# Kernel tuning notes

Measured on AMD Instinct MI355X. Metric: run time of the kernel, lower is better.

## Reference

```python
import jax, jax.numpy as jnp
import numpy as np

DIM, H, K, RADIUS = 128, 4, 32, 0.3
DH = DIM // H
N, M = 16384, 4096


def setup_inputs() -> dict:
    key = jax.random.key(0)
    ks = jax.random.split(key, 16)
    s = 0.02
    return {
        "xyz": jax.random.normal(ks[0], (N, 3), jnp.float32),
        "feats": jax.random.normal(ks[1], (N, DIM), jnp.float32),
        "idx_center": jax.random.randint(ks[2], (M,), 0, N, jnp.int64),
        "Wq": jax.random.normal(ks[3], (DIM, DIM), jnp.float32) * s,
        "Wk": jax.random.normal(ks[4], (DIM, DIM), jnp.float32) * s,
        "Wv": jax.random.normal(ks[5], (DIM, DIM), jnp.float32) * s,
        "Wo": jax.random.normal(ks[6], (DIM, DIM), jnp.float32) * s,
        "bo": jnp.zeros((DIM,), jnp.float32),
        "g1": jnp.ones((DIM,), jnp.float32),
        "be1": jnp.zeros((DIM,), jnp.float32),
        "g2": jnp.ones((DIM,), jnp.float32),
        "be2": jnp.zeros((DIM,), jnp.float32),
        "W1": jax.random.normal(ks[7], (4 * DIM, DIM), jnp.float32) * s,
        "b1f": jnp.zeros((4 * DIM,), jnp.float32),
        "W2": jax.random.normal(ks[8], (DIM, 4 * DIM), jnp.float32) * s,
        "b2f": jnp.zeros((DIM,), jnp.float32),
    }


def _layernorm(x, g, b, eps=1e-5):
    mu = x.mean(-1, keepdims=True)
    var = ((x - mu) ** 2).mean(-1, keepdims=True)
    return (x - mu) / jnp.sqrt(var + eps) * g + b


def reference(xyz, feats, idx_center, Wq, Wk, Wv, Wo, bo, g1, be1, g2, be2, W1, b1f, W2, b2f):
    m = idx_center.shape[0]
    c_xyz = xyz[idx_center]          # (M,3)
    c_feat = feats[idx_center]       # (M,DIM)
    # pairwise Euclidean distance (M,N), like torch.cdist
    d2 = (jnp.sum(c_xyz * c_xyz, -1)[:, None] + jnp.sum(xyz * xyz, -1)[None, :]
          - 2.0 * (c_xyz @ xyz.T))
    dist = jnp.sqrt(jnp.maximum(d2, 1e-12))
    mask = dist < RADIUS
    mask = mask.at[jnp.arange(m), idx_center].set(True)  # force self-inclusion
    dmask = jnp.where(mask, dist, jnp.inf)
    neg_d, nbr_idx = jax.lax.top_k(-dmask, K)            # k smallest distances
    nbr_dist = -neg_d
    valid = jnp.isfinite(nbr_dist)                       # (M,K)
    nbr_feats = jnp.where(valid[..., None], feats[nbr_idx], 0.0)  # (M,K,DIM)
    # tiny per-center attention
    q = (c_feat @ Wq.T).reshape(m, H, DH)
    k = (nbr_feats @ Wk.T).reshape(m, K, H, DH).transpose(0, 2, 1, 3)  # (M,H,K,DH)
    v = (nbr_feats @ Wv.T).reshape(m, K, H, DH).transpose(0, 2, 1, 3)
    attn = jnp.einsum('mhd,mhkd->mhk', q * (DH ** -0.5), k)
    attn = jnp.where(valid[:, None, :], attn, -1e9)
    attn = jax.nn.softmax(attn, axis=-1)
    out = jnp.einsum('mhk,mhkd->mhd', attn, v)
    out = out.transpose(0, 2, 1).reshape(m, DIM)  # matches torch transpose(1,2).reshape
    upd = out @ Wo.T + bo
    c_feat = c_feat + _layernorm(upd, g1, be1)
    ffn = jax.nn.relu(c_feat @ W1.T + b1f) @ W2.T + b2f
    c_feat = c_feat + _layernorm(ffn, g2, be2)
    nearest = jnp.argmin(dist, axis=0)            # (N,) nearest center per point
    return feats + c_feat[nearest]
```

## Files before the change

### kernel.cpp

```cpp
#include <hip/hip_runtime.h>
#include <hip/hip_bf16.h>

#define DIMF 128
#define KNBR 32
#define NH 4
#define DH 32
#define RADIUS 0.3f
#define CB 8
#define CAND 256
#define PPB 64
#define TMAIN 512

#define PACK_BLOCKS 60

typedef unsigned long long u64t;

__device__ __forceinline__ void tr4_tile(const float4* __restrict__ in4, float4* __restrict__ out4,
                                         int AI, int BI, int a0, int b0, int t, char* smem) {
    float4(*tile)[33] = (float4(*)[33])smem;
    int tx = t & 31, ty = t >> 5;
    for (int r = ty; r < 32; r += 8) tile[r][tx] = in4[(long)(b0 + r) * AI + a0 + tx];
    __syncthreads();
    for (int r = ty; r < 32; r += 8) out4[(long)(a0 + r) * BI + b0 + tx] = tile[tx][r];
}

__global__ __launch_bounds__(256) void pack_kernel(
    const float* __restrict__ Wq, const float* __restrict__ Wv,
    const float* __restrict__ Wo, const float* __restrict__ W1,
    const float* __restrict__ W2, const float* __restrict__ Wk,
    float4* __restrict__ qp4, float4* __restrict__ vp4, float4* __restrict__ op4,
    float4* __restrict__ w1p4, float4* __restrict__ w2p4, float4* __restrict__ kp4) {
    __shared__ __align__(16) char smem[16896];
    int pk = blockIdx.x, t = threadIdx.x;
    if (pk < 4) {
        tr4_tile((const float4*)Wq, qp4, 32, 128, 0, pk * 32, t, smem);
    } else if (pk < 8) {
        tr4_tile((const float4*)Wv, vp4, 32, 128, 0, (pk - 4) * 32, t, smem);
    } else if (pk < 12) {
        tr4_tile((const float4*)Wo, op4, 32, 128, 0, (pk - 8) * 32, t, smem);
    } else if (pk < 28) {
        tr4_tile((const float4*)W1, w1p4, 32, 512, 0, (pk - 12) * 32, t, smem);
    } else if (pk < 44) {
        int i = pk - 28;
        tr4_tile((const float4*)W2, w2p4, 128, 128, (i >> 2) * 32, (i & 3) * 32, t, smem);
    } else {
        int idx = (pk - 44) * 256 + t;
        int q = idx >> 7, j = idx & 127;
        float4 w;
        w.x = Wk[(long)(4 * q + 0) * DIMF + j];
        w.y = Wk[(long)(4 * q + 1) * DIMF + j];
        w.z = Wk[(long)(4 * q + 2) * DIMF + j];
        w.w = Wk[(long)(4 * q + 3) * DIMF + j];
        kp4[q * DIMF + j] = w;
    }
}

__global__ __launch_bounds__(512, 4) void main_kernel(
    const float* __restrict__ xyz, const float* __restrict__ feats,
    const int* __restrict__ idxc,
    const float4* __restrict__ qp4, const float4* __restrict__ kp4,
    const float4* __restrict__ vp4, const float4* __restrict__ op4,
    const float* __restrict__ bo, const float* __restrict__ g1,
    const float* __restrict__ be1, const float* __restrict__ g2,
    const float* __restrict__ be2, const float4* __restrict__ w1p4,
    const float* __restrict__ b1f, const float4* __restrict__ w2p4,
    const float* __restrict__ b2f, float* __restrict__ cfin,
    int* __restrict__ bestm, int N, int M) {
    __shared__ __align__(16) char smem[32768];
    __shared__ int nbrl[CB][KNBR];
    __shared__ int cnt[CB];

    int t = threadIdx.x;
    int b = blockIdx.x;
    int nAttn = M / CB;

    if (b >= nAttn) {
        float4* cds = (float4*)smem;
        int pt = t >> 3, q = t & 7;
        int n = (b - nAttn) * PPB + pt;
        float px = xyz[3 * n], py = xyz[3 * n + 1], pz = xyz[3 * n + 2];
        float bd0 = INFINITY, bd1 = INFINITY;
        int bm0 = 0, bm1 = 0;
        for (int c0 = 0; c0 < M; c0 += 1024) {
            __syncthreads();
            for (int i = t; i < 1024; i += TMAIN) {
                int ic = idxc[c0 + i];
                float cx = xyz[3 * ic], cy = xyz[3 * ic + 1], cz = xyz[3 * ic + 2];
                cds[i] = make_float4(-2.0f * cx, -2.0f * cy, -2.0f * cz,
                                     (cx * cx + cy * cy) + cz * cz);
            }
            __syncthreads();
#pragma unroll 8
            for (int i = 0; i < 64; ++i) {
                int ci0 = q + (2 * i) * 8, ci1 = q + (2 * i + 1) * 8;
                float4 ca = cds[ci0];
                float4 cb = cds[ci1];
                float sa = fmaf(ca.x, px, fmaf(ca.y, py, fmaf(ca.z, pz, ca.w)));
                float sb = fmaf(cb.x, px, fmaf(cb.y, py, fmaf(cb.z, pz, cb.w)));
                if (sa < bd0) { bd0 = sa; bm0 = c0 + ci0; }
                if (sb < bd1) { bd1 = sb; bm1 = c0 + ci1; }
            }
        }
        if (bd1 < bd0 || (bd1 == bd0 && bm1 < bm0)) { bd0 = bd1; bm0 = bm1; }
#pragma unroll
        for (int o = 1; o < 8; o <<= 1) {
            float obd = __shfl_xor(bd0, o);
            int obm = __shfl_xor(bm0, o);
            if (obd < bd0 || (obd == bd0 && obm < bm0)) { bd0 = obd; bm0 = obm; }
        }
        if (q == 0) bestm[n] = bm0;
        return;
    }

    int m0 = b * CB;

    {
        u64t(*cand)[CAND] = (u64t(*)[CAND])smem;
        if (t < CB) cnt[t] = 0;
        __syncthreads();
        float nx[CB], ny[CB], nz[CB], cw[CB];
#pragma unroll
        for (int tc = 0; tc < CB; ++tc) {
            int ic = idxc[m0 + tc];
            float cx = xyz[3 * ic], cy = xyz[3 * ic + 1], cz = xyz[3 * ic + 2];
            cw[tc] = (cx * cx + cy * cy) + cz * cz;
            nx[tc] = -2.0f * cx; ny[tc] = -2.0f * cy; nz[tc] = -2.0f * cz;
        }
        const float R2 = RADIUS * RADIUS;
        for (int n = t; n < N; n += TMAIN) {
            float x = xyz[3 * n], y = xyz[3 * n + 1], z = xyz[3 * n + 2];
            float pw = (x * x + y * y) + z * z;
            float rhs = R2 - pw;
#pragma unroll
            for (int tc = 0; tc < CB; ++tc) {
                float s = fmaf(nx[tc], x, fmaf(ny[tc], y, fmaf(nz[tc], z, cw[tc])));
                if (s < rhs) {
                    int pos = atomicAdd(&cnt[tc], 1);
                    if (pos < CAND)
                        cand[tc][pos] = (((u64t)__float_as_uint(fmaxf(s + pw, 0.0f))) << 32) | (unsigned)n;
                }
            }
        }
        __syncthreads();
        int w = t >> 6, lane = t & 63;
        {
            int cidx = w;
            int C = cnt[cidx] < CAND ? cnt[cidx] : CAND;
            const u64t* vc = cand[cidx];
            if (C <= 64) {
                u64t mykey = (lane < C) ? vc[lane] : ~0ull;
                int rank = 0;
                for (int j = 0; j < C; ++j) rank += (vc[j] < mykey) ? 1 : 0;
                if (lane < C && rank < KNBR) nbrl[cidx][rank] = (int)(mykey & 0xffffffffu);
                if (lane >= C && lane < KNBR) nbrl[cidx][lane] = -1;
            } else {
                u64t mykey[4];
                int myrank[4];
#pragma unroll
                for (int s = 0; s < 4; ++s) {
                    int i = s * 64 + lane;
                    mykey[s] = (i < C) ? vc[i] : ~0ull;
                    myrank[s] = 0;
                }
                for (int j = 0; j < C; ++j) {
                    u64t kj = vc[j];
#pragma unroll
                    for (int s = 0; s < 4; ++s) myrank[s] += (kj < mykey[s]) ? 1 : 0;
                }
#pragma unroll
                for (int s = 0; s < 4; ++s) {
                    int i = s * 64 + lane;
                    if (i < C && myrank[s] < KNBR) nbrl[cidx][myrank[s]] = (int)(mykey[s] & 0xffffffffu);
                }
            }
        }
    }
    __syncthreads();

    float(*cf)[DIMF] = (float(*)[DIMF])smem;
    float(*cf2)[DIMF] = (float(*)[DIMF])(smem + 4096);
    float(*S1)[4 * DIMF] = (float(*)[4 * DIMF])(smem + 8192);
    float(*S2)[DIMF] = (float(*)[DIMF])(smem + 24576);
    float(*S3)[DIMF] = (float(*)[DIMF])(smem + 28672);

    if (t < 256) {
        int c8t = t >> 5, k32t = t & 31;
        int ic = idxc[m0 + c8t];
        *(float4*)&cf[c8t][k32t * 4] = *(const float4*)&feats[(long)ic * DIMF + k32t * 4];
    }
    __syncthreads();

    {
        int i = t & 127, cpair = (t >> 7) * 2;
        float acc0 = 0.f, acc1 = 0.f;
        for (int jj = 0; jj < 32; ++jj) {
            float4 w = qp4[jj * DIMF + i];
            float4 x0 = *(const float4*)&cf[cpair][jj * 4];
            float4 x1 = *(const float4*)&cf[cpair + 1][jj * 4];
            acc0 += w.x * x0.x + w.y * x0.y + w.z * x0.z + w.w * x0.w;
            acc1 += w.x * x1.x + w.y * x1.y + w.z * x1.z + w.w * x1.w;
        }
        S2[cpair][i] = acc0 * 0.17677669529663687f;
        S2[cpair + 1][i] = acc1 * 0.17677669529663687f;
    }
    __syncthreads();

    {
        int j = t & 127, h = t >> 7;
        float acc[8] = {0.f, 0.f, 0.f, 0.f, 0.f, 0.f, 0.f, 0.f};
        for (int d4 = 0; d4 < 8; ++d4) {
            float4 w = kp4[(h * 8 + d4) * DIMF + j];
#pragma unroll
            for (int c = 0; c < 8; ++c) {
                float4 qv = *(const float4*)&S2[c][h * DH + d4 * 4];
                acc[c] += qv.x * w.x + qv.y * w.y + qv.z * w.z + qv.w * w.w;
            }
        }
#pragma unroll
        for (int c = 0; c < 8; ++c) S1[c][h * DIMF + j] = acc[c];
    }
    __syncthreads();

    {
        int c8 = t >> 6, hh = (t >> 5) & 1, k32 = t & 31;
        int h0 = hh * 2, h1 = hh * 2 + 1;
        int ni = nbrl[c8][k32];
        const float* nrow = feats + (long)(ni < 0 ? 0 : ni) * DIMF;
        float lg0 = 0.f, lg1 = 0.f;
        for (int jj = 0; jj < 32; ++jj) {
            float4 f = *(const float4*)&nrow[jj * 4];
            float4 qa = *(const float4*)&S1[c8][h0 * DIMF + jj * 4];
            float4 qb = *(const float4*)&S1[c8][h1 * DIMF + jj * 4];
            lg0 += f.x * qa.x + f.y * qa.y + f.z * qa.z + f.w * qa.w;
            lg1 += f.x * qb.x + f.y * qb.y + f.z * qb.z + f.w * qb.w;
        }
        if (ni < 0) { lg0 = -1e9f; lg1 = -1e9f; }
        {
            float mx = lg0;
            for (int o = 16; o; o >>= 1) mx = fmaxf(mx, __shfl_xor(mx, o, 32));
            float e = expf(lg0 - mx);
            float s = e;
            for (int o = 16; o; o >>= 1) s += __shfl_xor(s, o, 32);
            S3[c8][h0 * KNBR + k32] = e / s;
        }
        {
            float mx = lg1;
            for (int o = 16; o; o >>= 1) mx = fmaxf(mx, __shfl_xor(mx, o, 32));
            float e = expf(lg1 - mx);
            float s = e;
            for (int o = 16; o; o >>= 1) s += __shfl_xor(s, o, 32);
            S3[c8][h1 * KNBR + k32] = e / s;
        }
    }
    __syncthreads();

    {
        int c8 = t >> 6, hh = (t >> 5) & 1, j32 = t & 31;
        int j4 = j32 * 4;
        int h0 = hh * 2, h1 = hh * 2 + 1;
        float a0x = 0.f, a0y = 0.f, a0z = 0.f, a0w = 0.f;
        float a1x = 0.f, a1y = 0.f, a1z = 0.f, a1w = 0.f;
        for (int k = 0; k < KNBR; ++k) {
            int ni = nbrl[c8][k];
            const float* nrow = feats + (long)(ni < 0 ? 0 : ni) * DIMF;
            float4 f = *(const float4*)&nrow[j4];
            float w0 = S3[c8][h0 * KNBR + k], w1 = S3[c8][h1 * KNBR + k];
            a0x += w0 * f.x; a0y += w0 * f.y; a0z += w0 * f.z; a0w += w0 * f.w;
            a1x += w1 * f.x; a1y += w1 * f.y; a1z += w1 * f.z; a1w += w1 * f.w;
        }
        __syncthreads();
        *(float4*)&S1[c8][h0 * DIMF + j4] = make_float4(a0x, a0y, a0z, a0w);
        *(float4*)&S1[c8][h1 * DIMF + j4] = make_float4(a1x, a1y, a1z, a1w);
    }
    __syncthreads();

    {
        int i = t & 127, cpair = (t >> 7) * 2;
        int h = i >> 5, d = i & 31;
        float acc0 = 0.f, acc1 = 0.f;
        for (int jj = 0; jj < 32; ++jj) {
            float4 w = vp4[jj * DIMF + i];
            float4 p0 = *(const float4*)&S1[cpair][h * DIMF + jj * 4];
            float4 p1 = *(const float4*)&S1[cpair + 1][h * DIMF + jj * 4];
            acc0 += w.x * p0.x + w.y * p0.y + w.z * p0.z + w.w * p0.w;
            acc1 += w.x * p1.x + w.y * p1.y + w.z * p1.z + w.w * p1.w;
        }
        __syncthreads();
        S2[cpair][d * NH + h] = acc0;
        S2[cpair + 1][d * NH + h] = acc1;
    }
    __syncthreads();

    {
        int i = t & 127, cpair = (t >> 7) * 2;
        float acc0 = 0.f, acc1 = 0.f;
        for (int jj = 0; jj < 32; ++jj) {
            float4 w = op4[jj * DIMF + i];
            float4 x0 = *(const float4*)&S2[cpair][jj * 4];
            float4 x1 = *(const float4*)&S2[cpair + 1][jj * 4];
            acc0 += w.x * x0.x + w.y * x0.y + w.z * x0.z + w.w * x0.w;
            acc1 += w.x * x1.x + w.y * x1.y + w.z * x1.z + w.w * x1.w;
        }
        float bb = bo[i];
        __syncthreads();
        S3[cpair][i] = acc0 + bb;
        S3[cpair + 1][i] = acc1 + bb;
    }
    __syncthreads();

    if (t < 256) {
        int c8 = t >> 5, k32 = t & 31;
        int i4 = k32 * 4;
        float4 u = *(const float4*)&S3[c8][i4];
        float s = ((u.x + u.y) + u.z) + u.w;
        for (int o = 16; o; o >>= 1) s += __shfl_xor(s, o, 32);
        float mu = s * (1.0f / DIMF);
        float d0 = u.x - mu, d1 = u.y - mu, d2 = u.z - mu, d3 = u.w - mu;
        float vs = ((d0 * d0 + d1 * d1) + d2 * d2) + d3 * d3;
        for (int o = 16; o; o >>= 1) vs += __shfl_xor(vs, o, 32);
        float rs = 1.0f / sqrtf(vs * (1.0f / DIMF) + 1e-5f);
        float4 g = *(const float4*)&g1[i4];
        float4 b = *(const float4*)&be1[i4];
        float4 base = *(const float4*)&cf[c8][i4];
        float4 r;
        r.x = base.x + d0 * rs * g.x + b.x;
        r.y = base.y + d1 * rs * g.y + b.y;
        r.z = base.z + d2 * rs * g.z + b.z;
        r.w = base.w + d3 * rs * g.w + b.w;
        *(float4*)&cf2[c8][i4] = r;
    }
    __syncthreads();

    {
        int u0 = t & 127, p = t >> 7;
        int u = p * DIMF + u0;
        float acc[8] = {0.f, 0.f, 0.f, 0.f, 0.f, 0.f, 0.f, 0.f};
        for (int jj = 0; jj < 32; ++jj) {
            float4 w = w1p4[jj * 512 + u];
#pragma unroll
            for (int c = 0; c < 8; ++c) {
                float4 x = *(const float4*)&cf2[c][jj * 4];
                acc[c] += w.x * x.x + w.y * x.y + w.z * x.z + w.w * x.w;
            }
        }
        float bb = b1f[u];
#pragma unroll
        for (int c = 0; c < 8; ++c) S1[c][u] = fmaxf(acc[c] + bb, 0.f);
    }
    __syncthreads();

    {
        int i = t & 127, cpair = (t >> 7) * 2;
        float acc0 = 0.f, acc1 = 0.f;
        for (int uu = 0; uu < 128; ++uu) {
            float4 w = w2p4[uu * DIMF + i];
            float4 h0v = *(const float4*)&S1[cpair][uu * 4];
            float4 h1v = *(const float4*)&S1[cpair + 1][uu * 4];
            acc0 += w.x * h0v.x + w.y * h0v.y + w.z * h0v.z + w.w * h0v.w;
            acc1 += w.x * h1v.x + w.y * h1v.y + w.z * h1v.z + w.w * h1v.w;
        }
        float bb = b2f[i];
        __syncthreads();
        S3[cpair][i] = acc0 + bb;
        S3[cpair + 1][i] = acc1 + bb;
    }
    __syncthreads();

    if (t < 256) {
        int c8 = t >> 5, k32 = t & 31;
        int i4 = k32 * 4;
        float4 u = *(const float4*)&S3[c8][i4];
        float s = ((u.x + u.y) + u.z) + u.w;
        for (int o = 16; o; o >>= 1) s += __shfl_xor(s, o, 32);
        float mu = s * (1.0f / DIMF);
        float d0 = u.x - mu, d1 = u.y - mu, d2 = u.z - mu, d3 = u.w - mu;
        float vs = ((d0 * d0 + d1 * d1) + d2 * d2) + d3 * d3;
        for (int o = 16; o; o >>= 1) vs += __shfl_xor(vs, o, 32);
        float rs = 1.0f / sqrtf(vs * (1.0f / DIMF) + 1e-5f);
        float4 g = *(const float4*)&g2[i4];
        float4 b = *(const float4*)&be2[i4];
        float4 base = *(const float4*)&cf2[c8][i4];
        float4 r;
        r.x = base.x + d0 * rs * g.x + b.x;
        r.y = base.y + d1 * rs * g.y + b.y;
        r.z = base.z + d2 * rs * g.z + b.z;
        r.w = base.w + d3 * rs * g.w + b.w;
        *(float4*)&cfin[(long)(m0 + c8) * DIMF + i4] = r;
    }
}

__global__ __launch_bounds__(256) void out_kernel(const float4* __restrict__ feats4,
                                                  const float* __restrict__ cfin,
                                                  const int* __restrict__ bestm,
                                                  float4* __restrict__ out4, int total) {
    int idx = blockIdx.x * 256 + threadIdx.x;
    if (idx >= total) return;
    int n = idx >> 5, c = idx & 31;
    const float4* cf4 = (const float4*)cfin;
    float4 f = feats4[idx];
    float4 g = cf4[(long)bestm[n] * 32 + c];
    out4[idx] = make_float4(f.x + g.x, f.y + g.y, f.z + g.z, f.w + g.w);
}

extern "C" void kernel_launch(void* const* d_in, const int* in_sizes, int n_in,
                              void* d_out, int out_size, void* d_ws, size_t ws_size,
                              hipStream_t stream) {
    const float* xyz = (const float*)d_in[0];
    const float* feats = (const float*)d_in[1];
    const int* idxc = (const int*)d_in[2];
    const float* Wq = (const float*)d_in[3];
    const float* Wk = (const float*)d_in[4];
    const float* Wv = (const float*)d_in[5];
    const float* Wo = (const float*)d_in[6];
    const float* bo = (const float*)d_in[7];
    const float* g1 = (const float*)d_in[8];
    const float* be1 = (const float*)d_in[9];
    const float* g2 = (const float*)d_in[10];
    const float* be2 = (const float*)d_in[11];
    const float* W1 = (const float*)d_in[12];
    const float* b1f = (const float*)d_in[13];
    const float* W2 = (const float*)d_in[14];
    const float* b2f = (const float*)d_in[15];

    int N = in_sizes[0] / 3;
    int M = in_sizes[2];

    char* ws = (char*)d_ws;
    size_t off = 0;
    float* cfin = (float*)(ws + off); off += (size_t)M * DIMF * 4;
    int* bestm = (int*)(ws + off); off += (size_t)N * 4;
    float4* qp4 = (float4*)(ws + off); off += (size_t)DIMF * DIMF * 4;
    float4* vp4 = (float4*)(ws + off); off += (size_t)DIMF * DIMF * 4;
    float4* op4 = (float4*)(ws + off); off += (size_t)DIMF * DIMF * 4;
    float4* kp4 = (float4*)(ws + off); off += (size_t)DIMF * DIMF * 4;
    float4* w1p4 = (float4*)(ws + off); off += (size_t)4 * DIMF * DIMF * 4;
    float4* w2p4 = (float4*)(ws + off); off += (size_t)4 * DIMF * DIMF * 4;
    (void)ws_size; (void)n_in; (void)out_size;

    pack_kernel<<<PACK_BLOCKS, 256, 0, stream>>>(
        Wq, Wv, Wo, W1, W2, Wk, qp4, vp4, op4, w1p4, w2p4, kp4);
    main_kernel<<<M / CB + N / PPB, TMAIN, 0, stream>>>(
        xyz, feats, idxc, qp4, kp4, vp4, op4, bo, g1, be1, g2, be2,
        w1p4, b1f, w2p4, b2f, cfin, bestm, N, M);
    out_kernel<<<(N * DIMF / 4 + 255) / 256, 256, 0, stream>>>(
        (const float4*)feats, cfin, bestm, (float4*)d_out, N * DIMF / 4);
}
```

Before: 192.8 us.

## Halve main kernel block to 4 centers and 256 threads

Shrinks each attention block from 8 centers with 512 threads to 4 centers with 256 threads, halves shared memory, and halves points per block in the nearest-center path. The K-projection and FFN1 loops are remapped so each thread covers two heads or two hidden slices to keep full coverage with fewer threads. The aim is more blocks, better CU load balance and lighter per-block sync. The cost is half the weight reuse per block, so each weight element is fetched twice as often from cache.

Result: slower. 204.5 us (+6.1%).

```diff
diff --git a/kernel.cpp b/kernel.cpp
--- a/kernel.cpp
+++ b/kernel.cpp
@@ -6,10 +6,10 @@
 #define NH 4
 #define DH 32
 #define RADIUS 0.3f
-#define CB 8
+#define CB 4
 #define CAND 256
-#define PPB 64
-#define TMAIN 512
+#define PPB 32
+#define TMAIN 256
 
 #define PACK_BLOCKS 60
 
@@ -55,7 +55,7 @@
     }
 }
 
-__global__ __launch_bounds__(512, 4) void main_kernel(
+__global__ __launch_bounds__(256) void main_kernel(
     const float* __restrict__ xyz, const float* __restrict__ feats,
     const int* __restrict__ idxc,
     const float4* __restrict__ qp4, const float4* __restrict__ kp4,
@@ -66,7 +66,7 @@
     const float* __restrict__ b1f, const float4* __restrict__ w2p4,
     const float* __restrict__ b2f, float* __restrict__ cfin,
     int* __restrict__ bestm, int N, int M) {
-    __shared__ __align__(16) char smem[32768];
+    __shared__ __align__(16) char smem[16384];
     __shared__ int nbrl[CB][KNBR];
     __shared__ int cnt[CB];
 
@@ -178,15 +178,15 @@
     __syncthreads();
 
     float(*cf)[DIMF] = (float(*)[DIMF])smem;
-    float(*cf2)[DIMF] = (float(*)[DIMF])(smem + 4096);
-    float(*S1)[4 * DIMF] = (float(*)[4 * DIMF])(smem + 8192);
-    float(*S2)[DIMF] = (float(*)[DIMF])(smem + 24576);
-    float(*S3)[DIMF] = (float(*)[DIMF])(smem + 28672);
-
-    if (t < 256) {
-        int c8t = t >> 5, k32t = t & 31;
-        int ic = idxc[m0 + c8t];
-        *(float4*)&cf[c8t][k32t * 4] = *(const float4*)&feats[(long)ic * DIMF + k32t * 4];
+    float(*cf2)[DIMF] = (float(*)[DIMF])(smem + 2048);
+    float(*S1)[4 * DIMF] = (float(*)[4 * DIMF])(smem + 4096);
+    float(*S2)[DIMF] = (float(*)[DIMF])(smem + 12288);
+    float(*S3)[DIMF] = (float(*)[DIMF])(smem + 14336);
+
+    if (t < 128) {
+        int c4 = t >> 5, k32 = t & 31;
+        int ic = idxc[m0 + c4];
+        *(float4*)&cf[c4][k32 * 4] = *(const float4*)&feats[(long)ic * DIMF + k32 * 4];
     }
     __syncthreads();
 
@@ -206,31 +206,35 @@
     __syncthreads();
 
     {
-        int j = t & 127, h = t >> 7;
-        float acc[8] = {0.f, 0.f, 0.f, 0.f, 0.f, 0.f, 0.f, 0.f};
-        for (int d4 = 0; d4 < 8; ++d4) {
-            float4 w = kp4[(h * 8 + d4) * DIMF + j];
-#pragma unroll
-            for (int c = 0; c < 8; ++c) {
-                float4 qv = *(const float4*)&S2[c][h * DH + d4 * 4];
-                acc[c] += qv.x * w.x + qv.y * w.y + qv.z * w.z + qv.w * w.w;
-            }
-        }
-#pragma unroll
-        for (int c = 0; c < 8; ++c) S1[c][h * DIMF + j] = acc[c];
-    }
-    __syncthreads();
-
-    {
-        int c8 = t >> 6, hh = (t >> 5) & 1, k32 = t & 31;
+        int j = t & 127, hbase = (t >> 7) * 2;
+#pragma unroll
+        for (int hh = 0; hh < 2; ++hh) {
+            int h = hbase + hh;
+            float acc[CB] = {0.f, 0.f, 0.f, 0.f};
+            for (int d4 = 0; d4 < 8; ++d4) {
+                float4 w = kp4[(h * 8 + d4) * DIMF + j];
+#pragma unroll
+                for (int c = 0; c < CB; ++c) {
+                    float4 qv = *(const float4*)&S2[c][h * DH + d4 * 4];
+                    acc[c] += qv.x * w.x + qv.y * w.y + qv.z * w.z + qv.w * w.w;
+                }
+            }
+#pragma unroll
+            for (int c = 0; c < CB; ++c) S1[c][h * DIMF + j] = acc[c];
+        }
+    }
+    __syncthreads();
+
+    {
+        int c4 = t >> 6, hh = (t >> 5) & 1, k32 = t & 31;
         int h0 = hh * 2, h1 = hh * 2 + 1;
-        int ni = nbrl[c8][k32];
+        int ni = nbrl[c4][k32];
         const float* nrow = feats + (long)(ni < 0 ? 0 : ni) * DIMF;
         float lg0 = 0.f, lg1 = 0.f;
         for (int jj = 0; jj < 32; ++jj) {
             float4 f = *(const float4*)&nrow[jj * 4];
-            float4 qa = *(const float4*)&S1[c8][h0 * DIMF + jj * 4];
-            float4 qb = *(const float4*)&S1[c8][h1 * DIMF + jj * 4];
+            float4 qa = *(const float4*)&S1[c4][h0 * DIMF + jj * 4];
+            float4 qb = *(const float4*)&S1[c4][h1 * DIMF + jj * 4];
             lg0 += f.x * qa.x + f.y * qa.y + f.z * qa.z + f.w * qa.w;
             lg1 += f.x * qb.x + f.y * qb.y + f.z * qb.z + f.w * qb.w;
         }
@@ -241,7 +245,7 @@
             float e = expf(lg0 - mx);
             float s = e;
             for (int o = 16; o; o >>= 1) s += __shfl_xor(s, o, 32);
-            S3[c8][h0 * KNBR + k32] = e / s;
+            S3[c4][h0 * KNBR + k32] = e / s;
         }
         {
             float mx = lg1;
@@ -249,28 +253,28 @@
             float e = expf(lg1 - mx);
             float s = e;
             for (int o = 16; o; o >>= 1) s += __shfl_xor(s, o, 32);
-            S3[c8][h1 * KNBR + k32] = e / s;
-        }
-    }
-    __syncthreads();
-
-    {
-        int c8 = t >> 6, hh = (t >> 5) & 1, j32 = t & 31;
+            S3[c4][h1 * KNBR + k32] = e / s;
+        }
+    }
+    __syncthreads();
+
+    {
+        int c4 = t >> 6, hh = (t >> 5) & 1, j32 = t & 31;
         int j4 = j32 * 4;
         int h0 = hh * 2, h1 = hh * 2 + 1;
         float a0x = 0.f, a0y = 0.f, a0z = 0.f, a0w = 0.f;
         float a1x = 0.f, a1y = 0.f, a1z = 0.f, a1w = 0.f;
         for (int k = 0; k < KNBR; ++k) {
-            int ni = nbrl[c8][k];
+            int ni = nbrl[c4][k];
             const float* nrow = feats + (long)(ni < 0 ? 0 : ni) * DIMF;
             float4 f = *(const float4*)&nrow[j4];
-            float w0 = S3[c8][h0 * KNBR + k], w1 = S3[c8][h1 * KNBR + k];
+            float w0 = S3[c4][h0 * KNBR + k], w1 = S3[c4][h1 * KNBR + k];
             a0x += w0 * f.x; a0y += w0 * f.y; a0z += w0 * f.z; a0w += w0 * f.w;
             a1x += w1 * f.x; a1y += w1 * f.y; a1z += w1 * f.z; a1w += w1 * f.w;
         }
         __syncthreads();
-        *(float4*)&S1[c8][h0 * DIMF + j4] = make_float4(a0x, a0y, a0z, a0w);
-        *(float4*)&S1[c8][h1 * DIMF + j4] = make_float4(a1x, a1y, a1z, a1w);
+        *(float4*)&S1[c4][h0 * DIMF + j4] = make_float4(a0x, a0y, a0z, a0w);
+        *(float4*)&S1[c4][h1 * DIMF + j4] = make_float4(a1x, a1y, a1z, a1w);
     }
     __syncthreads();
 
@@ -308,10 +312,10 @@
     }
     __syncthreads();
 
-    if (t < 256) {
-        int c8 = t >> 5, k32 = t & 31;
+    if (t < 128) {
+        int c4 = t >> 5, k32 = t & 31;
         int i4 = k32 * 4;
-        float4 u = *(const float4*)&S3[c8][i4];
+        float4 u = *(const float4*)&S3[c4][i4];
         float s = ((u.x + u.y) + u.z) + u.w;
         for (int o = 16; o; o >>= 1) s += __shfl_xor(s, o, 32);
         float mu = s * (1.0f / DIMF);
@@ -321,31 +325,43 @@
         float rs = 1.0f / sqrtf(vs * (1.0f / DIMF) + 1e-5f);
         float4 g = *(const float4*)&g1[i4];
         float4 b = *(const float4*)&be1[i4];
-        float4 base = *(const float4*)&cf[c8][i4];
+        float4 base = *(const float4*)&cf[c4][i4];
         float4 r;
         r.x = base.x + d0 * rs * g.x + b.x;
         r.y = base.y + d1 * rs * g.y + b.y;
         r.z = base.z + d2 * rs * g.z + b.z;
         r.w = base.w + d3 * rs * g.w + b.w;
-        *(float4*)&cf2[c8][i4] = r;
-    }
-    __syncthreads();
-
-    {
-        int u0 = t & 127, p = t >> 7;
-        int u = p * DIMF + u0;
-        float acc[8] = {0.f, 0.f, 0.f, 0.f, 0.f, 0.f, 0.f, 0.f};
+        *(float4*)&cf2[c4][i4] = r;
+    }
+    __syncthreads();
+
+    {
+        int u0 = t & 127, pbase = t >> 7;
+        float acc[2][CB];
+#pragma unroll
+        for (int pp = 0; pp < 2; ++pp)
+#pragma unroll
+            for (int c = 0; c < CB; ++c) acc[pp][c] = 0.f;
         for (int jj = 0; jj < 32; ++jj) {
-            float4 w = w1p4[jj * 512 + u];
-#pragma unroll
-            for (int c = 0; c < 8; ++c) {
-                float4 x = *(const float4*)&cf2[c][jj * 4];
-                acc[c] += w.x * x.x + w.y * x.y + w.z * x.z + w.w * x.w;
-            }
-        }
-        float bb = b1f[u];
-#pragma unroll
-        for (int c = 0; c < 8; ++c) S1[c][u] = fmaxf(acc[c] + bb, 0.f);
+            float4 x[CB];
+#pragma unroll
+            for (int c = 0; c < CB; ++c) x[c] = *(const float4*)&cf2[c][jj * 4];
+#pragma unroll
+            for (int pp = 0; pp < 2; ++pp) {
+                int u = (pbase + pp * 2) * DIMF + u0;
+                float4 w = w1p4[jj * 512 + u];
+#pragma unroll
+                for (int c = 0; c < CB; ++c)
+                    acc[pp][c] += w.x * x[c].x + w.y * x[c].y + w.z * x[c].z + w.w * x[c].w;
+            }
+        }
+#pragma unroll
+        for (int pp = 0; pp < 2; ++pp) {
+            int u = (pbase + pp * 2) * DIMF + u0;
+            float bb = b1f[u];
+#pragma unroll
+            for (int c = 0; c < CB; ++c) S1[c][u] = fmaxf(acc[pp][c] + bb, 0.f);
+        }
     }
     __syncthreads();
 
@@ -366,10 +382,10 @@
     }
     __syncthreads();
 
-    if (t < 256) {
-        int c8 = t >> 5, k32 = t & 31;
+    if (t < 128) {
+        int c4 = t >> 5, k32 = t & 31;
         int i4 = k32 * 4;
-        float4 u = *(const float4*)&S3[c8][i4];
+        float4 u = *(const float4*)&S3[c4][i4];
         float s = ((u.x + u.y) + u.z) + u.w;
         for (int o = 16; o; o >>= 1) s += __shfl_xor(s, o, 32);
         float mu = s * (1.0f / DIMF);
@@ -379,13 +395,13 @@
         float rs = 1.0f / sqrtf(vs * (1.0f / DIMF) + 1e-5f);
         float4 g = *(const float4*)&g2[i4];
         float4 b = *(const float4*)&be2[i4];
-        float4 base = *(const float4*)&cf2[c8][i4];
+        float4 base = *(const float4*)&cf2[c4][i4];
         float4 r;
         r.x = base.x + d0 * rs * g.x + b.x;
         r.y = base.y + d1 * rs * g.y + b.y;
         r.z = base.z + d2 * rs * g.z + b.z;
         r.w = base.w + d3 * rs * g.w + b.w;
-        *(float4*)&cfin[(long)(m0 + c8) * DIMF + i4] = r;
+        *(float4*)&cfin[(long)(m0 + c4) * DIMF + i4] = r;
     }
 }
 
```
